# Kernel tuning notes

Hardware: AMD Instinct MI355X
Metric: run time of the kernel (lower is better)

The kernel has to match this reference:

```python
import jax, jax.numpy as jnp
import numpy as np

B, N, C = 8, 4096, 1024
H, D = 16, 64
FF = 4096
EPS_ATTN = 1e-6
EPS_LN = 1e-5


def layer_norm(x, g, b, eps=EPS_LN):
    mu = jnp.mean(x, axis=-1, keepdims=True)
    var = jnp.mean(jnp.square(x - mu), axis=-1, keepdims=True)
    return (x - mu) * jax.lax.rsqrt(var + eps) * g + b


def phi(x):
    # elu(x) + 1
    return jnp.where(x > 0, x + 1.0, jnp.exp(x))


def setup_inputs() -> dict:
    key = jax.random.key(0)
    ks = jax.random.split(key, 8)
    src = jax.random.normal(ks[0], (B, N, C), dtype=jnp.float32)
    lengths = jax.random.randint(ks[1], (B,), int(0.75 * N), N + 1)
    src_key_padding_mask = jnp.arange(N)[None, :] >= lengths[:, None]
    s = 0.02
    qkv_w = jax.random.normal(ks[2], (3 * C, C), dtype=jnp.float32) * s
    qkv_b = jnp.zeros((3 * C,), jnp.float32)
    out_w = jax.random.normal(ks[3], (C, C), dtype=jnp.float32) * s
    out_b = jnp.zeros((C,), jnp.float32)
    w1 = jax.random.normal(ks[4], (FF, C), dtype=jnp.float32) * s
    b1 = jnp.zeros((FF,), jnp.float32)
    w2 = jax.random.normal(ks[5], (C, FF), dtype=jnp.float32) * s
    b2 = jnp.zeros((C,), jnp.float32)
    ln1_g = jnp.ones((C,), jnp.float32)
    ln1_b = jnp.zeros((C,), jnp.float32)
    ln2_g = jnp.ones((C,), jnp.float32)
    ln2_b = jnp.zeros((C,), jnp.float32)
    return dict(src=src, src_key_padding_mask=src_key_padding_mask,
                qkv_w=qkv_w, qkv_b=qkv_b, out_w=out_w, out_b=out_b,
                w1=w1, b1=b1, w2=w2, b2=b2,
                ln1_g=ln1_g, ln1_b=ln1_b, ln2_g=ln2_g, ln2_b=ln2_b)


def linear_attention(x, mask, qkv_w, qkv_b, out_w, out_b):
    b, n, c = x.shape
    qkv = (x @ qkv_w.T + qkv_b).reshape(b, n, 3, H, D)
    qkv = jnp.transpose(qkv, (2, 0, 3, 1, 4))  # [3,B,H,N,D]
    q, k, v = qkv[0], qkv[1], qkv[2]
    qf, kf = phi(q), phi(k)
    valid = (~mask).astype(kf.dtype)[:, None, :, None]  # [B,1,N,1]
    kf = kf * valid
    v = v * valid
    kv = jnp.einsum('bhnd,bhne->bhde', kf, v)          # [B,H,D,D]
    z = kf.sum(axis=2)                                  # [B,H,D]
    y_num = jnp.einsum('bhnd,bhde->bhne', qf, kv)       # [B,H,N,D]
    y_den = jnp.maximum(jnp.einsum('bhnd,bhd->bhn', qf, z), EPS_ATTN)
    y = y_num / y_den[..., None]
    y = jnp.transpose(y, (0, 2, 1, 3)).reshape(b, n, c)
    return y @ out_w.T + out_b


def reference(src, src_key_padding_mask, qkv_w, qkv_b, out_w, out_b,
              w1, b1, w2, b2, ln1_g, ln1_b, ln2_g, ln2_b):
    # pre-norm: attention block
    attn_out = linear_attention(layer_norm(src, ln1_g, ln1_b), src_key_padding_mask,
                                qkv_w, qkv_b, out_w, out_b)
    x = src + attn_out
    # pre-norm: FFN block (exact gelu, matching torch F.gelu default)
    h = jax.nn.gelu(layer_norm(x, ln2_g, ln2_b) @ w1.T + b1, approximate=False)
    return x + (h @ w2.T + b2)
```

## Files before the change

kernel.cpp:

```cpp
#include <hip/hip_runtime.h>
#include <cmath>
#include <cstdint>

#define MTOK 32768
#define CDIM 1024
#define SEQ  4096
#define NHEAD 16
#define HDIM 64
#define FFDIM 4096

typedef __attribute__((ext_vector_type(8))) short short8;
typedef __attribute__((ext_vector_type(4))) float f32x4;

static __device__ __forceinline__ float b2f(unsigned short u){
  union { unsigned int i; float f; } c; c.i = ((unsigned int)u)<<16; return c.f;
}
static __device__ __forceinline__ unsigned short f2b(float f){
  union { float f; unsigned int i; } c; c.f = f;
  return (unsigned short)((c.i + 0x7fffu + ((c.i>>16)&1u)) >> 16);
}
static __device__ __forceinline__ float fast_gelu(float v){
  float s = v*0.70710678118654752f;
  float a = fabsf(s);
  float t = 1.f/(1.f + 0.3275911f*a);
  float p = t*(0.254829592f + t*(-0.284496736f + t*(1.421413741f +
            t*(-1.453152027f + t*1.061405429f))));
  float erfa = 1.f - p*__expf(-a*a);
  float er = (s<0.f)? -erfa : erfa;
  return 0.5f*v*(1.f+er);
}
static __device__ __forceinline__ void async16(const void* g, void* l){
  __builtin_amdgcn_global_load_lds((const __attribute__((address_space(1))) void*)g,
                                   (__attribute__((address_space(3))) void*)l, 16, 0, 0);
}

__global__ void detect_mask_kernel(const unsigned int* __restrict__ m, int* __restrict__ flag){
  __shared__ int any;
  if(threadIdx.x==0) any=0;
  __syncthreads();
  int loc=0;
  for(int i=threadIdx.x;i<8192;i+=256) if(m[i]>1u) loc=1;
  if(loc) atomicOr(&any,1);
  __syncthreads();
  if(threadIdx.x==0) *flag=any;
}
__global__ void decode_mask_kernel(const void* __restrict__ m, const int* __restrict__ flag,
                                   float* __restrict__ validf){
  int i = blockIdx.x*256 + threadIdx.x;
  int pad = (*flag) ? (int)((const unsigned char*)m)[i] : ((const int*)m)[i];
  validf[i] = pad ? 0.f : 1.f;
}

__global__ void cast_all_kernel(const float* __restrict__ a, const float* __restrict__ b,
                                const float* __restrict__ c, const float* __restrict__ d,
                                unsigned short* __restrict__ oa, unsigned short* __restrict__ ob,
                                unsigned short* __restrict__ oc, unsigned short* __restrict__ od){
  long i = ((long)blockIdx.x*256 + threadIdx.x)*4;
  const float* x; unsigned short* y; long off;
  if(i < 3145728){ x=a; y=oa; off=i; }
  else if(i < 4194304){ x=b; y=ob; off=i-3145728; }
  else if(i < 8388608){ x=c; y=oc; off=i-4194304; }
  else { x=d; y=od; off=i-8388608; }
  float4 v = *(const float4*)(x+off);
  ushort4 o; o.x=f2b(v.x); o.y=f2b(v.y); o.z=f2b(v.z); o.w=f2b(v.w);
  *(ushort4*)(y+off)=o;
}

__global__ __launch_bounds__(256) void ln_kernel(const float* __restrict__ x,
    const float* __restrict__ g, const float* __restrict__ bt, unsigned short* __restrict__ out){
  int row = blockIdx.x, t = threadIdx.x;
  const float* xr = x + (size_t)row*CDIM;
  float4 v = *(const float4*)(xr + t*4);
  float s1 = v.x+v.y+v.z+v.w;
  float s2 = v.x*v.x+v.y*v.y+v.z*v.z+v.w*v.w;
  #pragma unroll
  for(int off=32; off>0; off>>=1){ s1+=__shfl_down(s1,off); s2+=__shfl_down(s2,off); }
  __shared__ float a1[4], a2[4];
  __shared__ float mu_s, rs_s;
  if((t&63)==0){ a1[t>>6]=s1; a2[t>>6]=s2; }
  __syncthreads();
  if(t==0){
    float u1=a1[0]+a1[1]+a1[2]+a1[3], u2=a2[0]+a2[1]+a2[2]+a2[3];
    float mu=u1*(1.f/CDIM);
    mu_s=mu; rs_s=rsqrtf(u2*(1.f/CDIM)-mu*mu+1e-5f);
  }
  __syncthreads();
  float mu=mu_s, rs=rs_s;
  float4 gg=*(const float4*)(g+t*4), bb=*(const float4*)(bt+t*4);
  ushort4 o;
  o.x=f2b((v.x-mu)*rs*gg.x+bb.x);
  o.y=f2b((v.y-mu)*rs*gg.y+bb.y);
  o.z=f2b((v.z-mu)*rs*gg.z+bb.z);
  o.w=f2b((v.w-mu)*rs*gg.w+bb.w);
  *(ushort4*)(out+(size_t)row*CDIM+t*4)=o;
}

template<int MODE>
__global__ __launch_bounds__(256,2) void gemm_bt(
    const unsigned short* __restrict__ A, const unsigned short* __restrict__ Bw,
    const float* __restrict__ bias, const float* __restrict__ extra,
    float* __restrict__ Cf, unsigned short* __restrict__ Cb,
    unsigned short* __restrict__ Kt, unsigned short* __restrict__ Vt,
    int M, int N, int K)
{
  __shared__ __align__(16) unsigned short As[128*64];
  __shared__ __align__(16) unsigned short Bs[128*64];
  const int tid = threadIdx.x;
  const int wave = tid>>6, lane = tid&63;
  const int wm = wave>>1, wn = wave&1;
  const int gx  = gridDim.x;
  const int f   = blockIdx.y * gx + blockIdx.x;
  const int xcd = f & 7;
  const int kk  = f >> 3;
  const int idx = kk & 31, g = kk >> 5;
  const int nq  = gx >> 2;
  const int gxq = g % nq, gy = g / nq;
  const int nx  = gxq*4 + (idx>>3);
  const int ny  = (gy*8 + (idx&7))*8 + xcd;
  const int m0 = ny*128, n0 = nx*128;
  const int lrow = lane>>3;
  const int gcol = (((lane&7) ^ lrow))*8;

  f32x4 acc[4][4];
  #pragma unroll
  for(int i=0;i<4;i++)
    #pragma unroll
    for(int j=0;j<4;j++) acc[i][j]=(f32x4)(0.f);

  const int ar = wm*64 + (lane&15);
  const int br = wn*64 + (lane&15);
  const int kc = lane>>4;
  const int xorv = lane&7;

  for(int kt=0; kt<K; kt+=64){
    #pragma unroll
    for(int it=0; it<4; it++){
      int wo = wave*4+it;
      int r  = wo*8 + lrow;
      async16(A  + (size_t)(m0+r)*K + kt + gcol, (void*)&As[wo*512]);
      async16(Bw + (size_t)(n0+r)*K + kt + gcol, (void*)&Bs[wo*512]);
    }
    __syncthreads();
    #pragma unroll
    for(int ks=0; ks<2; ks++){
      const int ch = ((ks*4 + kc) ^ xorv)*8;
      short8 a[4], b[4];
      #pragma unroll
      for(int i=0;i<4;i++){
        a[i]=*(const short8*)&As[(ar+i*16)*64 + ch];
        b[i]=*(const short8*)&Bs[(br+i*16)*64 + ch];
      }
      #pragma unroll
      for(int i=0;i<4;i++)
        #pragma unroll
        for(int j=0;j<4;j++)
          acc[i][j]=__builtin_amdgcn_mfma_f32_16x16x32_bf16(a[i],b[j],acc[i][j],0,0,0);
    }
    __syncthreads();
  }
  const int rbase = m0 + wm*64 + (lane>>4)*4;
  const int cbase = n0 + wn*64 + (lane&15);
  if(MODE==0){
    #pragma unroll
    for(int mi=0;mi<4;mi++){
      int mrow = rbase + mi*16;
      float4 vld = *(const float4*)(extra + mrow);
      float vv[4] = {vld.x, vld.y, vld.z, vld.w};
      #pragma unroll
      for(int ni=0;ni<4;ni++){
        int n = cbase + ni*16;
        float bs = bias[n];
        int part = n>>10;
        if(part==0){
          #pragma unroll
          for(int i=0;i<4;i++){
            float v = acc[mi][ni][i] + bs;
            float p = (v>0.f)? (v+1.f) : __expf(v);
            Cb[(size_t)(mrow+i)*1024 + n] = f2b(p);
          }
        } else {
          int d = n & 63, hh = (n>>6) & 15;
          int bb_ = mrow >> 12, pos = mrow & 4095;
          unsigned short* dst = (part==1? Kt : Vt)
              + (((size_t)(bb_*16+hh)*64 + d)*SEQ + pos);
          ushort4 o;
          #pragma unroll
          for(int i=0;i<4;i++){
            float v = acc[mi][ni][i] + bs;
            float r = (part==1)? (((v>0.f)?(v+1.f):__expf(v))*vv[i]) : (v*vv[i]);
            ((unsigned short*)&o)[i] = f2b(r);
          }
          *(ushort4*)dst = o;
        }
      }
    }
  } else {
    #pragma unroll
    for(int mi=0;mi<4;mi++){
      #pragma unroll
      for(int i=0;i<4;i++){
        int m = rbase + mi*16 + i;
        #pragma unroll
        for(int ni=0;ni<4;ni++){
          int n = cbase + ni*16;
          float v = acc[mi][ni][i] + bias[n];
          if(MODE==1){
            size_t off=(size_t)m*N+n;
            Cf[off] = v + extra[off];
          } else if(MODE==2){
            Cb[(size_t)m*N+n] = f2b(fast_gelu(v));
          } else {
            size_t off=(size_t)m*N+n;
            Cf[off] += v;
          }
        }
      }
    }
  }
}

__global__ __launch_bounds__(64) void kvz_mfma_kernel(
    const unsigned short* __restrict__ Kt, const unsigned short* __restrict__ Vt,
    float* __restrict__ kvp, float* __restrict__ zp)
{
  __shared__ __align__(16) unsigned short Ks[2][64*64];
  __shared__ __align__(16) unsigned short Vs[2][64*64];
  const int blk = blockIdx.x;
  const int bh = blk>>4, kcn = blk&15;
  const int n0 = kcn*256;
  const int lane = threadIdx.x;
  const int r8 = lane>>3;
  const int gch = ((lane&7) ^ r8)*8;
  const size_t base = (size_t)bh*64*SEQ + n0 + gch;
  f32x4 acc[4][4];
  #pragma unroll
  for(int i=0;i<4;i++)
    #pragma unroll
    for(int j=0;j<4;j++) acc[i][j]=(f32x4)(0.f);
  float zacc[4]={0.f,0.f,0.f,0.f};
  const int l15 = lane&15, kc4 = lane>>4, x7 = lane&7;
  for(int rr=0; rr<2; rr++){
    if(rr) asm volatile("s_waitcnt lgkmcnt(0)" ::: "memory");
    #pragma unroll
    for(int t=0;t<2;t++){
      int cc = rr*2 + t;
      #pragma unroll
      for(int wo=0;wo<8;wo++){
        int r = wo*8 + r8;
        async16(Kt + base + (size_t)r*SEQ + cc*64, (void*)&Ks[t][wo*512]);
        async16(Vt + base + (size_t)r*SEQ + cc*64, (void*)&Vs[t][wo*512]);
      }
    }
    asm volatile("s_waitcnt vmcnt(0)" ::: "memory");
    #pragma unroll
    for(int t=0;t<2;t++){
      #pragma unroll
      for(int ks=0; ks<2; ks++){
        const int ch = ((ks*4 + kc4) ^ x7)*8;
        short8 a[4], b[4];
        #pragma unroll
        for(int i=0;i<4;i++) a[i]=*(const short8*)&Vs[t][(l15+i*16)*64 + ch];
        #pragma unroll
        for(int j=0;j<4;j++) b[j]=*(const short8*)&Ks[t][(l15+j*16)*64 + ch];
        #pragma unroll
        for(int j=0;j<4;j++)
          #pragma unroll
          for(int e8=0;e8<8;e8++) zacc[j] += b2f((unsigned short)b[j][e8]);
        #pragma unroll
        for(int i=0;i<4;i++)
          #pragma unroll
          for(int j=0;j<4;j++)
            acc[i][j]=__builtin_amdgcn_mfma_f32_16x16x32_bf16(a[i],b[j],acc[i][j],0,0,0);
      }
    }
  }
  #pragma unroll
  for(int j=0;j<4;j++){
    float v = zacc[j];
    v += __shfl_down(v, 32);
    v += __shfl_down(v, 16);
    if(lane<16) zp[(size_t)blk*64 + j*16 + lane] = v;
  }
  float* kvd = kvp + (size_t)blk*4096;
  #pragma unroll
  for(int i=0;i<4;i++)
    #pragma unroll
    for(int j=0;j<4;j++)
      #pragma unroll
      for(int r=0;r<4;r++)
        kvd[(i*16 + kc4*4 + r)*64 + j*16 + l15] = acc[i][j][r];
}

__global__ void kvz_reduce_kernel(const float* __restrict__ kvp, const float* __restrict__ zp,
                                  unsigned short* __restrict__ kvtb){
  int bh = blockIdx.x, t = threadIdx.x;
  for(int idx=t; idx<5120; idx+=256){
    int e = idx>>6, d = idx&63;
    float s = 0.f;
    if(e < 64){
      for(int c=0;c<16;c++) s += kvp[((size_t)bh*16+c)*4096 + e*64 + d];
    } else if(e == 64){
      for(int c=0;c<16;c++) s += zp[((size_t)bh*16+c)*64 + d];
    }
    kvtb[(size_t)bh*5120 + idx] = f2b(s);
  }
}

__global__ __launch_bounds__(256) void y_gemm_kernel(
    const unsigned short* __restrict__ qb, const unsigned short* __restrict__ kvtb,
    unsigned short* __restrict__ ybuf)
{
  __shared__ __align__(16) unsigned short As[128*64];
  __shared__ __align__(16) unsigned short Bs[80*64];
  const int tid = threadIdx.x, lane = tid&63, wave = tid>>6;
  const int bh = blockIdx.y, b = bh>>4, h = bh&15;
  const int m0 = blockIdx.x*128;
  const int r8 = lane>>3, gch = ((lane&7)^r8)*8;
  const unsigned short* qbase = qb + ((size_t)(b*SEQ + m0))*1024 + h*64 + gch;
  #pragma unroll
  for(int it=0; it<4; it++){
    int wo = wave*4 + it, r = wo*8 + r8;
    async16(qbase + (size_t)r*1024, (void*)&As[wo*512]);
  }
  const unsigned short* kvb = kvtb + (size_t)bh*5120 + gch;
  #pragma unroll
  for(int it=0; it<3; it++){
    int wo = wave + it*4;
    if(wo < 10){ int r = wo*8 + r8; async16(kvb + r*64, (void*)&Bs[wo*512]); }
  }
  __syncthreads();
  const int l15 = lane&15, kc4 = lane>>4, x7 = lane&7;
  f32x4 acc[2][5];
  #pragma unroll
  for(int i=0;i<2;i++)
    #pragma unroll
    for(int j=0;j<5;j++) acc[i][j]=(f32x4)(0.f);
  #pragma unroll
  for(int ks=0; ks<2; ks++){
    const int ch = ((ks*4 + kc4) ^ x7)*8;
    short8 a[2], bb[5];
    #pragma unroll
    for(int i=0;i<2;i++) a[i]=*(const short8*)&As[(wave*32 + i*16 + l15)*64 + ch];
    #pragma unroll
    for(int j=0;j<5;j++) bb[j]=*(const short8*)&Bs[(j*16 + l15)*64 + ch];
    #pragma unroll
    for(int i=0;i<2;i++)
      #pragma unroll
      for(int j=0;j<5;j++)
        acc[i][j]=__builtin_amdgcn_mfma_f32_16x16x32_bf16(a[i],bb[j],acc[i][j],0,0,0);
  }
  #pragma unroll
  for(int i=0;i<2;i++){
    #pragma unroll
    for(int r=0;r<4;r++){
      float den = __shfl(acc[i][4][r], lane & 48);
      float inv = 1.f/fmaxf(den, 1e-6f);
      size_t m = (size_t)(b*SEQ + m0 + wave*32 + i*16 + kc4*4 + r);
      #pragma unroll
      for(int j=0;j<4;j++)
        ybuf[m*1024 + h*64 + j*16 + l15] = f2b(acc[i][j][r]*inv);
    }
  }
}

extern "C" void kernel_launch(void* const* d_in, const int* in_sizes, int n_in,
                              void* d_out, int out_size, void* d_ws, size_t ws_size,
                              hipStream_t stream)
{
  const float* src   = (const float*)d_in[0];
  const void*  mask  = d_in[1];
  const float* qkv_w = (const float*)d_in[2];
  const float* qkv_b = (const float*)d_in[3];
  const float* out_w = (const float*)d_in[4];
  const float* out_b = (const float*)d_in[5];
  const float* w1    = (const float*)d_in[6];
  const float* b1    = (const float*)d_in[7];
  const float* w2    = (const float*)d_in[8];
  const float* b2    = (const float*)d_in[9];
  const float* ln1g  = (const float*)d_in[10];
  const float* ln1b  = (const float*)d_in[11];
  const float* ln2g  = (const float*)d_in[12];
  const float* ln2b  = (const float*)d_in[13];
  float* out = (float*)d_out;
  char* ws = (char*)d_ws;

  size_t o = 0;
  int* flag = (int*)(ws);                         o += 256;
  float* validf = (float*)(ws+o);                 o += (size_t)MTOK*4;
  unsigned short* wqb = (unsigned short*)(ws+o);  o += (size_t)3072*1024*2;
  unsigned short* wob = (unsigned short*)(ws+o);  o += (size_t)1024*1024*2;
  unsigned short* w1b = (unsigned short*)(ws+o);  o += (size_t)4096*1024*2;
  unsigned short* w2b = (unsigned short*)(ws+o);  o += (size_t)1024*4096*2;
  unsigned short* bufA = (unsigned short*)(ws+o); o += (size_t)MTOK*1024*2;
  char* R = ws+o;                                 o += (size_t)MTOK*4096*2;
  unsigned short* qb  = (unsigned short*)R;
  unsigned short* ktb = (unsigned short*)(R + (size_t)MTOK*1024*2);
  unsigned short* vtb = (unsigned short*)(R + (size_t)MTOK*2048*2);
  float* kvp = (float*)(R + (size_t)MTOK*3072*2);
  unsigned short* hbuf = (unsigned short*)R;
  float* zp = (float*)(ws+o);                     o += (size_t)2048*64*4;
  unsigned short* kvtb = (unsigned short*)(ws+o); o += (size_t)128*5120*2;

  detect_mask_kernel<<<1,256,0,stream>>>((const unsigned int*)mask, flag);
  decode_mask_kernel<<<MTOK/256,256,0,stream>>>(mask, flag, validf);
  cast_all_kernel<<<12288,256,0,stream>>>(qkv_w, out_w, w1, w2, wqb, wob, w1b, w2b);

  ln_kernel<<<MTOK,256,0,stream>>>(src, ln1g, ln1b, bufA);
  gemm_bt<0><<<dim3(3072/128, MTOK/128),256,0,stream>>>(bufA, wqb, qkv_b, validf, nullptr, qb, ktb, vtb, MTOK,3072,1024);
  kvz_mfma_kernel<<<2048,64,0,stream>>>(ktb, vtb, kvp, zp);
  kvz_reduce_kernel<<<128,256,0,stream>>>(kvp, zp, kvtb);
  y_gemm_kernel<<<dim3(SEQ/128,128),256,0,stream>>>(qb, kvtb, bufA);
  gemm_bt<1><<<dim3(1024/128, MTOK/128),256,0,stream>>>(bufA, wob, out_b, src, out, nullptr, nullptr, nullptr, MTOK,1024,1024);
  ln_kernel<<<MTOK,256,0,stream>>>(out, ln2g, ln2b, bufA);
  gemm_bt<2><<<dim3(4096/128, MTOK/128),256,0,stream>>>(bufA, w1b, b1, nullptr, nullptr, hbuf, nullptr, nullptr, MTOK,4096,1024);
  gemm_bt<3><<<dim3(1024/128, MTOK/128),256,0,stream>>>(hbuf, w2b, b2, nullptr, out, nullptr, nullptr, nullptr, MTOK,1024,4096);
}
```

Before: 1.320 ms.

## Switch GEMM inner loop to 32x32x16 bf16 MFMA and raise occupancy

Replaces the 16x16x32 MFMA tiling (4x4 accumulators per wave) with 32x32x16 MFMA (2x2 f32x16 accumulators), which cuts the number of LDS fragment loads per MFMA. The epilogue index mapping is rewritten to match the 32x32 output layout, and the launch bounds ask for 4 blocks per SM instead of 2. The main risks are register pressure from the tighter occupancy target, which could cause spills, and LDS bank conflicts from the new read pattern.

```diff
diff --git a/kernel.cpp b/kernel.cpp
--- a/kernel.cpp
+++ b/kernel.cpp
@@ -11,6 +11,7 @@
 
 typedef __attribute__((ext_vector_type(8))) short short8;
 typedef __attribute__((ext_vector_type(4))) float f32x4;
+typedef __attribute__((ext_vector_type(16))) float f32x16;
 
 static __device__ __forceinline__ float b2f(unsigned short u){
   union { unsigned int i; float f; } c; c.i = ((unsigned int)u)<<16; return c.f;
@@ -96,7 +97,7 @@
 }
 
 template<int MODE>
-__global__ __launch_bounds__(256,2) void gemm_bt(
+__global__ __launch_bounds__(256,4) void gemm_bt(
     const unsigned short* __restrict__ A, const unsigned short* __restrict__ Bw,
     const float* __restrict__ bias, const float* __restrict__ extra,
     float* __restrict__ Cf, unsigned short* __restrict__ Cb,
@@ -121,15 +122,15 @@
   const int lrow = lane>>3;
   const int gcol = (((lane&7) ^ lrow))*8;
 
-  f32x4 acc[4][4];
-  #pragma unroll
-  for(int i=0;i<4;i++)
-    #pragma unroll
-    for(int j=0;j<4;j++) acc[i][j]=(f32x4)(0.f);
-
-  const int ar = wm*64 + (lane&15);
-  const int br = wn*64 + (lane&15);
-  const int kc = lane>>4;
+  f32x16 acc[2][2];
+  #pragma unroll
+  for(int i=0;i<2;i++)
+    #pragma unroll
+    for(int j=0;j<2;j++) acc[i][j]=(f32x16)(0.f);
+
+  const int ar = wm*64 + (lane&31);
+  const int br = wn*64 + (lane&31);
+  const int kg = lane>>5;
   const int xorv = lane&7;
 
   for(int kt=0; kt<K; kt+=64){
@@ -142,68 +143,69 @@
     }
     __syncthreads();
     #pragma unroll
-    for(int ks=0; ks<2; ks++){
-      const int ch = ((ks*4 + kc) ^ xorv)*8;
-      short8 a[4], b[4];
-      #pragma unroll
-      for(int i=0;i<4;i++){
-        a[i]=*(const short8*)&As[(ar+i*16)*64 + ch];
-        b[i]=*(const short8*)&Bs[(br+i*16)*64 + ch];
-      }
-      #pragma unroll
-      for(int i=0;i<4;i++)
-        #pragma unroll
-        for(int j=0;j<4;j++)
-          acc[i][j]=__builtin_amdgcn_mfma_f32_16x16x32_bf16(a[i],b[j],acc[i][j],0,0,0);
+    for(int t=0; t<4; t++){
+      const int ch = ((2*t + kg) ^ xorv)*8;
+      short8 a0 = *(const short8*)&As[(ar   )*64 + ch];
+      short8 a1 = *(const short8*)&As[(ar+32)*64 + ch];
+      short8 b0 = *(const short8*)&Bs[(br   )*64 + ch];
+      short8 b1 = *(const short8*)&Bs[(br+32)*64 + ch];
+      acc[0][0]=__builtin_amdgcn_mfma_f32_32x32x16_bf16(a0,b0,acc[0][0],0,0,0);
+      acc[0][1]=__builtin_amdgcn_mfma_f32_32x32x16_bf16(a0,b1,acc[0][1],0,0,0);
+      acc[1][0]=__builtin_amdgcn_mfma_f32_32x32x16_bf16(a1,b0,acc[1][0],0,0,0);
+      acc[1][1]=__builtin_amdgcn_mfma_f32_32x32x16_bf16(a1,b1,acc[1][1],0,0,0);
     }
     __syncthreads();
   }
-  const int rbase = m0 + wm*64 + (lane>>4)*4;
-  const int cbase = n0 + wn*64 + (lane&15);
+  const int col5 = lane&31;
+  const int rhi  = 4*(lane>>5);
   if(MODE==0){
     #pragma unroll
-    for(int mi=0;mi<4;mi++){
-      int mrow = rbase + mi*16;
-      float4 vld = *(const float4*)(extra + mrow);
-      float vv[4] = {vld.x, vld.y, vld.z, vld.w};
-      #pragma unroll
-      for(int ni=0;ni<4;ni++){
-        int n = cbase + ni*16;
-        float bs = bias[n];
-        int part = n>>10;
-        if(part==0){
-          #pragma unroll
-          for(int i=0;i<4;i++){
-            float v = acc[mi][ni][i] + bs;
-            float p = (v>0.f)? (v+1.f) : __expf(v);
-            Cb[(size_t)(mrow+i)*1024 + n] = f2b(p);
+    for(int am=0;am<2;am++){
+      #pragma unroll
+      for(int q=0;q<4;q++){
+        int mrow = m0 + wm*64 + am*32 + q*8 + rhi;
+        float4 vld = *(const float4*)(extra + mrow);
+        float vv[4] = {vld.x, vld.y, vld.z, vld.w};
+        #pragma unroll
+        for(int bn=0;bn<2;bn++){
+          int n = n0 + wn*64 + bn*32 + col5;
+          float bs = bias[n];
+          int part = n>>10;
+          if(part==0){
+            #pragma unroll
+            for(int i=0;i<4;i++){
+              float v = acc[am][bn][q*4+i] + bs;
+              float p = (v>0.f)? (v+1.f) : __expf(v);
+              Cb[(size_t)(mrow+i)*1024 + n] = f2b(p);
+            }
+          } else {
+            int d = n & 63, hh = (n>>6) & 15;
+            int bb_ = mrow >> 12, pos = mrow & 4095;
+            unsigned short* dst = (part==1? Kt : Vt)
+                + (((size_t)(bb_*16+hh)*64 + d)*SEQ + pos);
+            ushort4 o;
+            #pragma unroll
+            for(int i=0;i<4;i++){
+              float v = acc[am][bn][q*4+i] + bs;
+              float r = (part==1)? (((v>0.f)?(v+1.f):__expf(v))*vv[i]) : (v*vv[i]);
+              ((unsigned short*)&o)[i] = f2b(r);
+            }
+            *(ushort4*)dst = o;
           }
-        } else {
-          int d = n & 63, hh = (n>>6) & 15;
-          int bb_ = mrow >> 12, pos = mrow & 4095;
-          unsigned short* dst = (part==1? Kt : Vt)
-              + (((size_t)(bb_*16+hh)*64 + d)*SEQ + pos);
-          ushort4 o;
-          #pragma unroll
-          for(int i=0;i<4;i++){
-            float v = acc[mi][ni][i] + bs;
-            float r = (part==1)? (((v>0.f)?(v+1.f):__expf(v))*vv[i]) : (v*vv[i]);
-            ((unsigned short*)&o)[i] = f2b(r);
-          }
-          *(ushort4*)dst = o;
         }
       }
     }
   } else {
     #pragma unroll
-    for(int mi=0;mi<4;mi++){
-      #pragma unroll
-      for(int i=0;i<4;i++){
-        int m = rbase + mi*16 + i;
-        #pragma unroll
-        for(int ni=0;ni<4;ni++){
-          int n = cbase + ni*16;
-          float v = acc[mi][ni][i] + bias[n];
+    for(int am=0;am<2;am++){
+      #pragma unroll
+      for(int bn=0;bn<2;bn++){
+        int n = n0 + wn*64 + bn*32 + col5;
+        float bs = bias[n];
+        #pragma unroll
+        for(int reg=0;reg<16;reg++){
+          int m = m0 + wm*64 + am*32 + (reg&3) + 8*(reg>>2) + rhi;
+          float v = acc[am][bn][reg] + bs;
           if(MODE==1){
             size_t off=(size_t)m*N+n;
             Cf[off] = v + extra[off];
```

Result: slower. 1.456 ms (+10.3%).
